# Performance work log

Hardware: AMD Instinct MI355X
Metric: run time of the kernel (lower is better)

The kernel has to match this reference:

```python
import jax, jax.numpy as jnp
import numpy as np

DIM = 2048
N_HEADS = 16
N_KV_HEADS = 8
HEAD_DIM = DIM // N_HEADS  # 128
N_REP = N_HEADS // N_KV_HEADS  # 2
B, L = 2, 2048
ROPE_THETA = 10000.0


def make_freqs_cis(L, head_dim, theta):
    inv = 1.0 / (theta ** (np.arange(0, head_dim, 2, dtype=np.float32) / head_dim))
    t = np.arange(L, dtype=np.float32)
    ang = np.outer(t, inv)  # [L, head_dim//2]
    return jnp.asarray(np.stack([np.cos(ang), np.sin(ang)], axis=-1))  # [L, hd//2, 2]


def setup_inputs() -> dict:
    key = jax.random.key(0)
    ks = jax.random.split(key, 5)
    s = 1.0 / np.sqrt(DIM)
    return {
        "x": jax.random.normal(ks[0], (B, L, DIM), dtype=jnp.float32),
        "freqs_cis": make_freqs_cis(L, HEAD_DIM, ROPE_THETA),
        "wq": jax.random.normal(ks[1], (DIM, N_HEADS * HEAD_DIM), dtype=jnp.float32) * s,
        "wk": jax.random.normal(ks[2], (DIM, N_KV_HEADS * HEAD_DIM), dtype=jnp.float32) * s,
        "wv": jax.random.normal(ks[3], (DIM, N_KV_HEADS * HEAD_DIM), dtype=jnp.float32) * s,
        "wo": jax.random.normal(ks[4], (N_HEADS * HEAD_DIM, DIM), dtype=jnp.float32) * s,
    }


def apply_rotary(x, freqs_cis):
    # x: [B, L, H, D]; freqs_cis: [L, D//2, 2] (cos, sin)
    xr = x.reshape(*x.shape[:-1], -1, 2)  # [B,L,H,D//2,2]
    cos = freqs_cis[None, :, None, :, 0]
    sin = freqs_cis[None, :, None, :, 1]
    out_r = xr[..., 0] * cos - xr[..., 1] * sin
    out_i = xr[..., 0] * sin + xr[..., 1] * cos
    return jnp.stack([out_r, out_i], axis=-1).reshape(x.shape).astype(x.dtype)


def reference(x, freqs_cis, wq, wk, wv, wo):
    Bx, Lx, _ = x.shape
    xq = (x @ wq).reshape(Bx, Lx, N_HEADS, HEAD_DIM)
    xk = (x @ wk).reshape(Bx, Lx, N_KV_HEADS, HEAD_DIM)
    xv = (x @ wv).reshape(Bx, Lx, N_KV_HEADS, HEAD_DIM)
    xq = apply_rotary(xq, freqs_cis)
    xk = apply_rotary(xk, freqs_cis)
    # repeat kv heads (GQA) then put heads first: [B, H, L, D]
    keys = jnp.repeat(xk, N_REP, axis=2).transpose(0, 2, 1, 3)
    values = jnp.repeat(xv, N_REP, axis=2).transpose(0, 2, 1, 3)
    xq = xq.transpose(0, 2, 1, 3)
    scores = jnp.einsum("bhqd,bhkd->bhqk", xq, keys) / jnp.sqrt(
        jnp.asarray(HEAD_DIM, dtype=xq.dtype))
    causal = jnp.tril(jnp.ones((Lx, Lx), dtype=bool))
    scores = jnp.where(causal[None, None], scores, -jnp.inf)
    probs = jax.nn.softmax(scores.astype(jnp.float32), axis=-1).astype(xq.dtype)
    out = jnp.einsum("bhqk,bhkd->bhqd", probs, values)
    out = out.transpose(0, 2, 1, 3).reshape(Bx, Lx, -1)
    return out @ wo
```

## Files before the change

kernel.cpp:

```cpp
#include <hip/hip_runtime.h>
#include <math.h>

typedef unsigned short u16;
typedef unsigned int   u32;
typedef u16   u16x8 __attribute__((ext_vector_type(8)));
typedef u16   u16x4 __attribute__((ext_vector_type(4)));
typedef u16   u16x2 __attribute__((ext_vector_type(2)));
typedef __bf16 bf16x8 __attribute__((ext_vector_type(8)));
typedef float  f32x4 __attribute__((ext_vector_type(4)));

__device__ __forceinline__ u16 f2b(float f) {
    union { float f; u32 u; } v; v.f = f;
    u32 u = v.u;
    return (u16)((u + 0x7FFFu + ((u >> 16) & 1u)) >> 16);
}

__device__ __forceinline__ void glds16(const void* g, void* l) {
    __builtin_amdgcn_global_load_lds(
        (__attribute__((address_space(1))) void*)(void*)g,
        (__attribute__((address_space(3))) void*)l, 16, 0, 0);
}

__global__ __launch_bounds__(256) void prep(
    const float* __restrict__ x, u16* __restrict__ Xb,
    const float* __restrict__ wq, const float* __restrict__ wk,
    const float* __restrict__ wv, const float* __restrict__ wo,
    u16* __restrict__ WT, u16* __restrict__ WOT)
{
    __shared__ u16 tile[64 * 72];
    const int t = threadIdx.x;
    const int bid = blockIdx.x;
    if (bid < 4096) {
        const size_t i = ((size_t)bid * 256 + t) * 8;
        f32x4 a = *(const f32x4*)&x[i];
        f32x4 b = *(const f32x4*)&x[i + 4];
        u16x8 o;
        #pragma unroll
        for (int j = 0; j < 4; ++j) { o[j] = f2b(a[j]); o[4 + j] = f2b(b[j]); }
        *(u16x8*)&Xb[i] = o;
        return;
    }
    const int tb = bid - 4096;
    const int bxx = tb % 96, by = tb / 96;
    const float* src; u16* dst; int cb, C;
    if (bxx < 32)      { src = wq; dst = WT;               cb = bxx;      C = 2048; }
    else if (bxx < 48) { src = wk; dst = WT + 2048 * 2048; cb = bxx - 32; C = 1024; }
    else if (bxx < 64) { src = wv; dst = WT + 3072 * 2048; cb = bxx - 48; C = 1024; }
    else               { src = wo; dst = WOT;              cb = bxx - 64; C = 2048; }
    const int r0 = by * 64, c0 = cb * 64;
    #pragma unroll
    for (int i = 0; i < 2; ++i) {
        int idx = i * 256 + t;
        int r = idx >> 3, c8 = (idx & 7) * 8;
        const float* sp = &src[(size_t)(r0 + r) * C + c0 + c8];
        f32x4 a = *(const f32x4*)sp;
        f32x4 b = *(const f32x4*)(sp + 4);
        u16x8 v;
        #pragma unroll
        for (int j = 0; j < 4; ++j) { v[j] = f2b(a[j]); v[4 + j] = f2b(b[j]); }
        *(u16x8*)&tile[r * 72 + c8] = v;
    }
    __syncthreads();
    #pragma unroll
    for (int i = 0; i < 2; ++i) {
        int idx = i * 256 + t;
        int orow = idx >> 3, oc8 = (idx & 7) * 8;
        u16x8 w;
        #pragma unroll
        for (int j = 0; j < 8; ++j) w[j] = tile[(oc8 + j) * 72 + orow];
        *(u16x8*)&dst[(size_t)(c0 + orow) * 2048 + r0 + oc8] = w;
    }
}

template <int MODE>
__global__ __launch_bounds__(256) void gemm_bt(
    const u16* __restrict__ A, const u16* __restrict__ Bt,
    u16* __restrict__ D0, u16* __restrict__ D1, u16* __restrict__ D2,
    float* __restrict__ Fout, const float* __restrict__ fc)
{
    __shared__ u16 Alds[128 * 32];
    __shared__ u16 Blds[128 * 32];
    const int t = threadIdx.x;
    const int wid = t >> 6, lane = t & 63;
    const int l15 = lane & 15, qd = lane >> 4;
    const int row0 = blockIdx.y * 128, col0 = blockIdx.x * 128;
    const int wm = (wid >> 1) * 64, wn = (wid & 1) * 64;

    const int sm = lane >> 2;
    const int sk = (lane & 3) * 8;
    const int c0 = wid * 2;
    const u16* Ag0 = A  + (size_t)(row0 + c0 * 16 + sm) * 2048 + sk;
    const u16* Ag1 = A  + (size_t)(row0 + (c0 + 1) * 16 + sm) * 2048 + sk;
    const u16* Bg0 = Bt + (size_t)(col0 + c0 * 16 + sm) * 2048 + sk;
    const u16* Bg1 = Bt + (size_t)(col0 + (c0 + 1) * 16 + sm) * 2048 + sk;
    u16* Al0 = Alds + c0 * 512; u16* Al1 = Alds + (c0 + 1) * 512;
    u16* Bl0 = Blds + c0 * 512; u16* Bl1 = Blds + (c0 + 1) * 512;

    f32x4 acc[4][4] = {};

    for (int k0 = 0; k0 < 2048; k0 += 32) {
        glds16(Ag0 + k0, Al0);
        glds16(Ag1 + k0, Al1);
        glds16(Bg0 + k0, Bl0);
        glds16(Bg1 + k0, Bl1);
        __syncthreads();
        bf16x8 af[4], bfr[4];
        #pragma unroll
        for (int mt = 0; mt < 4; ++mt)
            af[mt] = *(const bf16x8*)&Alds[(wm + mt * 16 + l15) * 32 + qd * 8];
        #pragma unroll
        for (int nt = 0; nt < 4; ++nt)
            bfr[nt] = *(const bf16x8*)&Blds[(wn + nt * 16 + l15) * 32 + qd * 8];
        __builtin_amdgcn_s_setprio(1);
        #pragma unroll
        for (int mt = 0; mt < 4; ++mt)
            #pragma unroll
            for (int nt = 0; nt < 4; ++nt)
                acc[mt][nt] = __builtin_amdgcn_mfma_f32_16x16x32_bf16(
                    af[mt], bfr[nt], acc[mt][nt], 0, 0, 0);
        __builtin_amdgcn_s_setprio(0);
        __syncthreads();
    }

    #pragma unroll
    for (int mt = 0; mt < 4; ++mt)
        #pragma unroll
        for (int nt = 0; nt < 4; ++nt) {
            const int gcol = col0 + wn + nt * 16 + l15;
            const int grow0 = row0 + wm + mt * 16 + qd * 4;
            if (MODE == 1) {
                #pragma unroll
                for (int r = 0; r < 4; ++r)
                    Fout[(size_t)(grow0 + r) * 2048 + gcol] = acc[mt][nt][r];
            } else if (gcol >= 3072) {
                const int vcol = gcol - 3072;
                const int vrow = vcol + (grow0 >> 11) * 1024;
                u16x4 v;
                #pragma unroll
                for (int r = 0; r < 4; ++r) v[r] = f2b(acc[mt][nt][r]);
                *(u16x4*)&D2[(size_t)vrow * 2048 + (grow0 & 2047)] = v;
            } else {
                const int p2 = gcol & 126;
                #pragma unroll
                for (int r = 0; r < 4; ++r) {
                    const int l = (grow0 + r) & 2047;
                    const float c = fc[l * 128 + p2];
                    const float s = fc[l * 128 + p2 + 1];
                    const float own = acc[mt][nt][r];
                    const float oth = __shfl_xor(own, 1);
                    const float rot = (l15 & 1) ? (oth * s + own * c)
                                                : (own * c - oth * s);
                    const u16 v = f2b(rot);
                    if (gcol < 2048)
                        D0[(size_t)(grow0 + r) * 2048 + gcol] = v;
                    else
                        D1[(size_t)(grow0 + r) * 1024 + (gcol - 2048)] = v;
                }
            }
        }
}

__global__ __launch_bounds__(256, 2) void attn_kernel(
    const u16* __restrict__ Q, const u16* __restrict__ K,
    const u16* __restrict__ Vt, u16* __restrict__ AO)
{
    __shared__ u16 SM[40960];
    const int t = threadIdx.x;
    const int w = t >> 6, lane = t & 63;
    const int l15 = lane & 15, qd = lane >> 4;
    const int b = blockIdx.x >> 3, kvh = blockIdx.x & 7;
    const int y = (int)blockIdx.y;
    const int qt = (y < 16) ? (31 - y) : (y - 16);
    const int h = kvh * 2 + (w >> 1);
    const float SCL = 0.08838834764831845f * 1.4426950408889634f;

    u16* K0 = SM;
    u16* K1 = SM + 8192;
    u16* V0 = SM + 16384;
    u16* V1 = SM + 24576;
    u16* PW = SM + 32768 + w * 2048;

    bf16x8 qf[2][4];
    #pragma unroll
    for (int mt = 0; mt < 2; ++mt) {
        const size_t grow = (size_t)b * 2048 + qt * 64 + (w & 1) * 32 + mt * 16 + l15;
        const u16* qp = Q + grow * 2048 + h * 128 + qd * 8;
        #pragma unroll
        for (int ks = 0; ks < 4; ++ks)
            qf[mt][ks] = *(const bf16x8*)(qp + ks * 32);
    }
    f32x4 Oa[2][8] = {};
    f32x4 Ls[2] = {};
    bf16x8 onesv;
    #pragma unroll
    for (int j = 0; j < 8; ++j) onesv[j] = (__bf16)1.0f;

    const u16* Kbase = K  + (size_t)b * 2048 * 1024 + kvh * 128;
    const u16* Vbase = Vt + (size_t)(b * 8 + kvh) * 128 * 2048;

    #pragma unroll
    for (int j = 0; j < 4; ++j) {
        const int f = w * 4 + j;
        glds16(Kbase + (size_t)((f >> 2) * 16 + l15) * 1024 + ((f & 3) * 4 + qd) * 8,
               K0 + f * 512);
        glds16(Vbase + (size_t)((f >> 1) * 16 + l15) * 2048 + ((f & 1) * 4 + qd) * 8,
               V0 + f * 512);
    }
    __syncthreads();

    for (int kt = 0; kt <= qt; ++kt) {
        u16* Kc = (kt & 1) ? K1 : K0;
        u16* Kn = (kt & 1) ? K0 : K1;
        u16* Vc = (kt & 1) ? V1 : V0;
        u16* Vn = (kt & 1) ? V0 : V1;
        if (kt < qt) {
            #pragma unroll
            for (int j = 0; j < 4; ++j) {
                const int f = w * 4 + j;
                glds16(Kbase + (size_t)((kt + 1) * 64 + (f >> 2) * 16 + l15) * 1024
                             + ((f & 3) * 4 + qd) * 8,
                       Kn + f * 512);
                glds16(Vbase + (size_t)((f >> 1) * 16 + l15) * 2048 + (kt + 1) * 64
                             + ((f & 1) * 4 + qd) * 8,
                       Vn + f * 512);
            }
        }

        f32x4 S[2][4] = {};
        #pragma unroll
        for (int ks = 0; ks < 4; ++ks) {
            bf16x8 bk[4];
            #pragma unroll
            for (int nt = 0; nt < 4; ++nt)
                bk[nt] = *(const bf16x8*)&Kc[(nt * 4 + ks) * 512 + lane * 8];
            __builtin_amdgcn_s_setprio(1);
            #pragma unroll
            for (int mt = 0; mt < 2; ++mt)
                #pragma unroll
                for (int nt = 0; nt < 4; ++nt)
                    S[mt][nt] = __builtin_amdgcn_mfma_f32_16x16x32_bf16(
                        qf[mt][ks], bk[nt], S[mt][nt], 0, 0, 0);
            __builtin_amdgcn_s_setprio(0);
        }
        if (kt == qt) {
            #pragma unroll
            for (int mt = 0; mt < 2; ++mt)
                #pragma unroll
                for (int r = 0; r < 4; ++r) {
                    const int qg = (w & 1) * 32 + mt * 16 + qd * 4 + r;
                    #pragma unroll
                    for (int nt = 0; nt < 4; ++nt)
                        if (nt * 16 + l15 > qg) S[mt][nt][r] = -__builtin_inff();
                }
        }
        #pragma unroll
        for (int mt = 0; mt < 2; ++mt)
            #pragma unroll
            for (int nt = 0; nt < 4; ++nt)
                #pragma unroll
                for (int r = 0; r < 4; ++r) {
                    const float p = exp2f(S[mt][nt][r] * SCL - 12.0f);
                    PW[(mt * 2 + (nt >> 1)) * 512 + ((nt * 2 + (l15 >> 3)) & 3) * 128
                       + (qd * 4 + r) * 8 + (l15 & 7)] = f2b(p);
                }

        #pragma unroll
        for (int ks = 0; ks < 2; ++ks) {
            bf16x8 pa[2], vb[8];
            #pragma unroll
            for (int mt = 0; mt < 2; ++mt)
                pa[mt] = *(const bf16x8*)&PW[(mt * 2 + ks) * 512 + lane * 8];
            #pragma unroll
            for (int nt = 0; nt < 8; ++nt)
                vb[nt] = *(const bf16x8*)&Vc[(nt * 2 + ks) * 512 + lane * 8];
            __builtin_amdgcn_s_setprio(1);
            #pragma unroll
            for (int mt = 0; mt < 2; ++mt) {
                Ls[mt] = __builtin_amdgcn_mfma_f32_16x16x32_bf16(
                    pa[mt], onesv, Ls[mt], 0, 0, 0);
                #pragma unroll
                for (int nt = 0; nt < 8; ++nt)
                    Oa[mt][nt] = __builtin_amdgcn_mfma_f32_16x16x32_bf16(
                        pa[mt], vb[nt], Oa[mt][nt], 0, 0, 0);
            }
            __builtin_amdgcn_s_setprio(0);
        }
        __syncthreads();
    }

    u16* OL = SM;
    #pragma unroll
    for (int mt = 0; mt < 2; ++mt)
        #pragma unroll
        for (int r = 0; r < 4; ++r) {
            const float inv = 1.f / Ls[mt][r];
            const int qr = (w & 1) * 32 + mt * 16 + qd * 4 + r;
            #pragma unroll
            for (int nt = 0; nt < 8; ++nt)
                OL[qr * 256 + (w >> 1) * 128 + nt * 16 + l15] = f2b(Oa[mt][nt][r] * inv);
        }
    __syncthreads();
    #pragma unroll
    for (int i = 0; i < 8; ++i) {
        const int c = i * 256 + t;
        const int row = c >> 5, ch = c & 31;
        u16x8 v = *(const u16x8*)&OL[row * 256 + ch * 8];
        *(u16x8*)&AO[((size_t)b * 2048 + qt * 64 + row) * 2048 + kvh * 256 + ch * 8] = v;
    }
}

extern "C" void kernel_launch(void* const* d_in, const int* in_sizes, int n_in,
                              void* d_out, int out_size, void* d_ws, size_t ws_size,
                              hipStream_t stream)
{
    (void)in_sizes; (void)n_in; (void)out_size; (void)ws_size;
    const float* x  = (const float*)d_in[0];
    const float* fc = (const float*)d_in[1];
    const float* wq = (const float*)d_in[2];
    const float* wk = (const float*)d_in[3];
    const float* wv = (const float*)d_in[4];
    const float* wo = (const float*)d_in[5];
    float* out = (float*)d_out;
    char* ws = (char*)d_ws;

    u16* Qb  = (u16*)(ws);
    u16* Kb  = (u16*)(ws + 16777216);
    u16* Vt  = (u16*)(ws + 25165824);
    u16* Xb  = (u16*)(ws + 33554432);
    u16* AO  = (u16*)(ws + 33554432);
    u16* WT  = (u16*)(ws + 50331648);
    u16* WOT = (u16*)(ws + 67108864);

    prep<<<4096 + 96 * 32, 256, 0, stream>>>(x, Xb, wq, wk, wv, wo, WT, WOT);

    gemm_bt<0><<<dim3(32, 32), 256, 0, stream>>>(Xb, WT, Qb, Kb, Vt, nullptr, fc);

    attn_kernel<<<dim3(16, 32), 256, 0, stream>>>(Qb, Kb, Vt, AO);

    gemm_bt<1><<<dim3(16, 32), 256, 0, stream>>>(AO, WOT, nullptr, nullptr, nullptr, out, nullptr);
}
```

Baseline: 258.6 us.

## Split GEMM K dimension across two wave groups with LDS reduction

The GEMM kernel now launches 512 threads per block, split into two groups of four waves. Each group handles half of the K range in its own LDS buffers, and the second group's accumulators are then reduced through shared memory into the first group's. This is meant to double the waves per tile to hide latency and raise MFMA occupancy on the under-occupied grids, especially the 512-block output projection. The cost is a 64KB LDS footprint, which may limit blocks per CU, plus an extra reduction pass through LDS.

```diff
diff --git a/kernel.cpp b/kernel.cpp
--- a/kernel.cpp
+++ b/kernel.cpp
@@ -73,32 +73,38 @@
 }
 
 template <int MODE>
-__global__ __launch_bounds__(256) void gemm_bt(
+__global__ __launch_bounds__(512) void gemm_bt(
     const u16* __restrict__ A, const u16* __restrict__ Bt,
     u16* __restrict__ D0, u16* __restrict__ D1, u16* __restrict__ D2,
     float* __restrict__ Fout, const float* __restrict__ fc)
 {
-    __shared__ u16 Alds[128 * 32];
-    __shared__ u16 Blds[128 * 32];
+    __shared__ __align__(16) char SMEM[65536];
     const int t = threadIdx.x;
     const int wid = t >> 6, lane = t & 63;
+    const int g  = wid >> 2;
+    const int w4 = wid & 3;
     const int l15 = lane & 15, qd = lane >> 4;
     const int row0 = blockIdx.y * 128, col0 = blockIdx.x * 128;
-    const int wm = (wid >> 1) * 64, wn = (wid & 1) * 64;
+    const int wm = (w4 >> 1) * 64, wn = (w4 & 1) * 64;
+
+    u16* SAg = (u16*)(SMEM + g * 8192);
+    u16* SBg = (u16*)(SMEM + 16384 + g * 8192);
+    float* RED = (float*)SMEM;
 
     const int sm = lane >> 2;
     const int sk = (lane & 3) * 8;
-    const int c0 = wid * 2;
-    const u16* Ag0 = A  + (size_t)(row0 + c0 * 16 + sm) * 2048 + sk;
-    const u16* Ag1 = A  + (size_t)(row0 + (c0 + 1) * 16 + sm) * 2048 + sk;
-    const u16* Bg0 = Bt + (size_t)(col0 + c0 * 16 + sm) * 2048 + sk;
-    const u16* Bg1 = Bt + (size_t)(col0 + (c0 + 1) * 16 + sm) * 2048 + sk;
-    u16* Al0 = Alds + c0 * 512; u16* Al1 = Alds + (c0 + 1) * 512;
-    u16* Bl0 = Blds + c0 * 512; u16* Bl1 = Blds + (c0 + 1) * 512;
+    const int c0 = w4 * 2;
+    const int kb = g * 1024;
+    const u16* Ag0 = A  + (size_t)(row0 + c0 * 16 + sm) * 2048 + kb + sk;
+    const u16* Ag1 = A  + (size_t)(row0 + (c0 + 1) * 16 + sm) * 2048 + kb + sk;
+    const u16* Bg0 = Bt + (size_t)(col0 + c0 * 16 + sm) * 2048 + kb + sk;
+    const u16* Bg1 = Bt + (size_t)(col0 + (c0 + 1) * 16 + sm) * 2048 + kb + sk;
+    u16* Al0 = SAg + c0 * 512; u16* Al1 = SAg + (c0 + 1) * 512;
+    u16* Bl0 = SBg + c0 * 512; u16* Bl1 = SBg + (c0 + 1) * 512;
 
     f32x4 acc[4][4] = {};
 
-    for (int k0 = 0; k0 < 2048; k0 += 32) {
+    for (int k0 = 0; k0 < 1024; k0 += 32) {
         glds16(Ag0 + k0, Al0);
         glds16(Ag1 + k0, Al1);
         glds16(Bg0 + k0, Bl0);
@@ -107,10 +113,10 @@
         bf16x8 af[4], bfr[4];
         #pragma unroll
         for (int mt = 0; mt < 4; ++mt)
-            af[mt] = *(const bf16x8*)&Alds[(wm + mt * 16 + l15) * 32 + qd * 8];
+            af[mt] = *(const bf16x8*)&SAg[(wm + mt * 16 + l15) * 32 + qd * 8];
         #pragma unroll
         for (int nt = 0; nt < 4; ++nt)
-            bfr[nt] = *(const bf16x8*)&Blds[(wn + nt * 16 + l15) * 32 + qd * 8];
+            bfr[nt] = *(const bf16x8*)&SBg[(wn + nt * 16 + l15) * 32 + qd * 8];
         __builtin_amdgcn_s_setprio(1);
         #pragma unroll
         for (int mt = 0; mt < 4; ++mt)
@@ -121,6 +127,27 @@
         __builtin_amdgcn_s_setprio(0);
         __syncthreads();
     }
+
+    if (g == 1) {
+        #pragma unroll
+        for (int mt = 0; mt < 4; ++mt)
+            #pragma unroll
+            for (int nt = 0; nt < 4; ++nt)
+                #pragma unroll
+                for (int r = 0; r < 4; ++r)
+                    RED[w4 * 4096 + (mt * 16 + qd * 4 + r) * 64 + nt * 16 + l15]
+                        = acc[mt][nt][r];
+    }
+    __syncthreads();
+    if (g == 1) return;
+    #pragma unroll
+    for (int mt = 0; mt < 4; ++mt)
+        #pragma unroll
+        for (int nt = 0; nt < 4; ++nt)
+            #pragma unroll
+            for (int r = 0; r < 4; ++r)
+                acc[mt][nt][r]
+                    += RED[w4 * 4096 + (mt * 16 + qd * 4 + r) * 64 + nt * 16 + l15];
 
     #pragma unroll
     for (int mt = 0; mt < 4; ++mt)
@@ -333,9 +360,9 @@
 
     prep<<<4096 + 96 * 32, 256, 0, stream>>>(x, Xb, wq, wk, wv, wo, WT, WOT);
 
-    gemm_bt<0><<<dim3(32, 32), 256, 0, stream>>>(Xb, WT, Qb, Kb, Vt, nullptr, fc);
+    gemm_bt<0><<<dim3(32, 32), 512, 0, stream>>>(Xb, WT, Qb, Kb, Vt, nullptr, fc);
 
     attn_kernel<<<dim3(16, 32), 256, 0, stream>>>(Qb, Kb, Vt, AO);
 
-    gemm_bt<1><<<dim3(16, 32), 256, 0, stream>>>(AO, WOT, nullptr, nullptr, nullptr, out, nullptr);
-}
+    gemm_bt<1><<<dim3(16, 32), 512, 0, stream>>>(AO, WOT, nullptr, nullptr, nullptr, out, nullptr);
+}
```

New measurement: 283.0 us. +9.5%, slower.
